# Kernel optimization log

Hardware: AMD Instinct MI355X
Metric: run time of the kernel (lower is better)

## Reference

```python
import jax, jax.numpy as jnp
import numpy as np

MASK_VALUE = -1000000000.0
N = 100000        # num nodes
E = 1600000       # num edges
IN_DIM = 128
HID = 128
MAXN = 100000     # max_num_nodes
TAU = 0.5


def setup_inputs() -> dict:
    key = jax.random.key(0)
    ks = jax.random.split(key, 24)
    s_in = 1.0 / np.sqrt(IN_DIM)
    s_h = 1.0 / np.sqrt(HID)
    s_2h = 1.0 / np.sqrt(2 * HID)
    return {
        "x": jax.random.normal(ks[0], (N, IN_DIM), jnp.float32),
        "edge_index": jax.random.randint(ks[1], (2, E), 0, N, jnp.int32),
        # GCN layer params (PyG GCNConv: lin weight + bias)
        "W1": jax.random.normal(ks[2], (IN_DIM, HID), jnp.float32) * s_in,
        "b1": jnp.zeros((HID,), jnp.float32),
        "W2": jax.random.normal(ks[3], (HID, HID), jnp.float32) * s_h,
        "b2": jnp.zeros((HID,), jnp.float32),
        "W3": jax.random.normal(ks[4], (HID, HID), jnp.float32) * s_h,
        "b3": jnp.zeros((HID,), jnp.float32),
        # heads
        "n1W": jax.random.normal(ks[5], (2 * HID, MAXN), jnp.float32) * s_2h,
        "n1b": jnp.zeros((MAXN,), jnp.float32),
        "n2W": jax.random.normal(ks[6], (2 * HID, MAXN), jnp.float32) * s_2h,
        "n2b": jnp.zeros((MAXN,), jnp.float32),
        "eW": jax.random.normal(ks[7], (2 * HID, 3), jnp.float32) * s_2h,
        "eb": jnp.zeros((3,), jnp.float32),
        "sW": jax.random.normal(ks[8], (2 * HID, 1), jnp.float32) * s_2h,
        "sb": jnp.zeros((1,), jnp.float32),
        # gumbel noise for the 4 gumbel_softmax calls (deterministic reference)
        "g1": jax.random.gumbel(ks[9], (1, MAXN), jnp.float32),
        "g2": jax.random.gumbel(ks[10], (1, MAXN), jnp.float32),
        "ge": jax.random.gumbel(ks[11], (1, 3), jnp.float32),
        "gs": jax.random.gumbel(ks[12], (1, 1), jnp.float32),
    }


def _gcn_layer(x, W, b, src, dst, n):
    # PyG GCNConv: self-loops + symmetric norm D^-1/2 (A+I) D^-1/2 (XW) + b
    h = x @ W                                            # [n, H]
    deg = jnp.zeros((n,), h.dtype).at[dst].add(1.0) + 1.0  # +1 self-loop
    dinv = jax.lax.rsqrt(deg)
    msg = h[src] * (dinv[src] * dinv[dst])[:, None]      # [E, H] gather
    out = jax.ops.segment_sum(msg, dst, num_segments=n)  # scatter-add at targets
    out = out + h * (dinv * dinv)[:, None]               # self-loop contribution
    return out + b


def _gumbel_softmax(logits, g):
    return jax.nn.softmax((logits + g) / TAU, axis=-1)


def _mask_logits(logits, n, prev_idx, src, dst):
    # logits: [1, MAXN]
    idx = jnp.arange(logits.shape[-1])
    logits = jnp.where(idx[None, :] >= n, MASK_VALUE, logits)
    if prev_idx is not None:
        m = (src == prev_idx) | (dst == prev_idx)
        conn = jnp.zeros((logits.shape[-1],), bool)
        # scatter True at connected nodes; unmatched edges map onto prev_idx
        conn = conn.at[jnp.where(m, src, prev_idx)].set(True)
        conn = conn.at[jnp.where(m, dst, prev_idx)].set(True)
        conn = conn.at[prev_idx].set(True)
        logits = jnp.where(conn[None, :], MASK_VALUE, logits)
    return logits


def reference(x, edge_index, W1, b1, W2, b2, W3, b3, n1W, n1b, n2W, n2b, eW, eb, sW, sb, g1, g2, ge, gs):
    src, dst = edge_index[0], edge_index[1]
    n = x.shape[0]
    h = jax.nn.relu(_gcn_layer(x, W1, b1, src, dst, n))
    h = jax.nn.relu(_gcn_layer(h, W2, b2, src, dst, n))
    gcn = jax.nn.relu(_gcn_layer(h, W3, b3, src, dst, n))   # [n, H]

    pool = jnp.concatenate([gcn.mean(0, keepdims=True), gcn.max(0, keepdims=True)], axis=1)  # [1, 2H]

    l1 = _mask_logits(pool @ n1W + n1b, n, None, src, dst)
    n1_soft = _gumbel_softmax(l1, g1)                      # [1, MAXN]
    i1 = jnp.argmax(n1_soft, axis=-1)[0]

    l2 = _mask_logits(pool @ n2W + n2b, n, i1, src, dst)
    n2_soft = _gumbel_softmax(l2, g2)
    i2 = jnp.argmax(n2_soft, axis=-1)[0]

    node_emb = jnp.concatenate([gcn[i1][None, :], gcn[i2][None, :]], axis=1)  # [1, 2H]
    e_soft = _gumbel_softmax(node_emb @ eW + eb, ge)       # [1, 3]
    s_soft = _gumbel_softmax(pool @ sW + sb, gs)           # [1, 1]
    return (n1_soft, n2_soft, e_soft, s_soft)
```

## Files before the change

kernel.cpp:

```cpp
#include <hip/hip_runtime.h>

#define HID 128
#define MASKV -1000000000.0f
#define INV_TAU 2.0f
#define NB_SHIFT 9
#define NBMAX 256
#define ECHUNK 4096
#define FP8_SCALE 16.0f
#define FP8_INV_SCALE 0.0625f

using short8 = __attribute__((ext_vector_type(8))) short;
using f32x4  = __attribute__((ext_vector_type(4))) float;
using f32x2  = __attribute__((ext_vector_type(2))) float;

__device__ inline ushort f2bf(float f) {
  unsigned u = __float_as_uint(f);
  return (ushort)((u + 0x7FFFu + ((u >> 16) & 1u)) >> 16);
}
__device__ inline float bflo(unsigned u) { return __uint_as_float(u << 16); }
__device__ inline float bfhi(unsigned u) { return __uint_as_float(u & 0xFFFF0000u); }

__device__ inline unsigned char f2fp8(float v) {
  int p = __builtin_amdgcn_cvt_pk_fp8_f32(v, v, 0, false);
  return (unsigned char)(p & 0xFF);
}
__device__ inline void acc_fp8x4(unsigned w, float& a0, float& a1, float& a2, float& a3) {
  f32x2 lo = __builtin_amdgcn_cvt_pk_f32_fp8((int)w, false);
  f32x2 hi = __builtin_amdgcn_cvt_pk_f32_fp8((int)w, true);
  a0 += lo[0]; a1 += lo[1]; a2 += hi[0]; a3 += hi[1];
}

__device__ inline unsigned ordered_bits(float f) {
  unsigned u = __float_as_uint(f);
  return (u & 0x80000000u) ? ~u : (u | 0x80000000u);
}
__device__ inline int key_idx(unsigned long long k) {
  return (int)(0xFFFFFFFFu - (unsigned)(k & 0xFFFFFFFFull));
}

__global__ __launch_bounds__(256) void zerok(uint4* __restrict__ p, int n16) {
  int i = blockIdx.x * 256 + threadIdx.x;
  if (i < n16) p[i] = make_uint4(0u, 0u, 0u, 0u);
}

__global__ __launch_bounds__(256) void cvt_w(const float* __restrict__ W1, const float* __restrict__ W2,
                                             const float* __restrict__ W3, ushort* __restrict__ Wt) {
  const float* W = (blockIdx.y == 0) ? W1 : (blockIdx.y == 1) ? W2 : W3;
  ushort* o = Wt + (size_t)blockIdx.y * 128 * 128;
  int idx = blockIdx.x * 256 + threadIdx.x;
  int c = idx >> 7, k = idx & 127;
  o[idx] = f2bf(W[k * 128 + c]);
}

__global__ __launch_bounds__(256) void bucket_count(const int* __restrict__ dst, int E, int* __restrict__ bcnt) {
  __shared__ int h[NBMAX];
  int t = threadIdx.x;
  h[t] = 0;
  __syncthreads();
  for (long long i = (long long)blockIdx.x * 256 + t; i < E; i += (long long)gridDim.x * 256) {
    atomicAdd(&h[dst[i] >> NB_SHIFT], 1);
  }
  __syncthreads();
  if (h[t]) atomicAdd(&bcnt[t], h[t]);
}

__global__ __launch_bounds__(256) void bucket_scan(const int* __restrict__ bcnt, int* __restrict__ bbase,
                                                   int* __restrict__ bcur, int nb, int E) {
  __shared__ int sh[256];
  int t = threadIdx.x;
  int v = (t < nb) ? bcnt[t] : 0;
  sh[t] = v;
  __syncthreads();
  for (int d = 1; d < 256; d <<= 1) {
    int x = (t >= d) ? sh[t - d] : 0;
    __syncthreads();
    sh[t] += x;
    __syncthreads();
  }
  int excl = sh[t] - v;
  if (t < nb) { bbase[t] = excl; bcur[t] = excl; }
  if (t == 0) bbase[nb] = E;
}

__global__ __launch_bounds__(256) void edge_bucket(const int* __restrict__ ei, int E, int nb,
                                                   int* __restrict__ bcur, int2* __restrict__ staged) {
  __shared__ int ssrc[ECHUNK];
  __shared__ int sdst[ECHUNK];
  __shared__ int hist[NBMAX];
  __shared__ int cur[NBMAX];
  int t = threadIdx.x;
  int e0 = blockIdx.x * ECHUNK;
  int cnt = min(ECHUNK, E - e0);
  if (t < nb) hist[t] = 0;
  __syncthreads();
  for (int i = t; i < cnt; i += 256) {
    ssrc[i] = ei[e0 + i];
    int d = ei[E + e0 + i];
    sdst[i] = d;
    atomicAdd(&hist[d >> NB_SHIFT], 1);
  }
  __syncthreads();
  if (t < nb) cur[t] = atomicAdd(&bcur[t], hist[t]);
  __syncthreads();
  for (int i = t; i < cnt; i += 256) {
    int d = sdst[i];
    int pos = atomicAdd(&cur[d >> NB_SHIFT], 1);
    staged[pos] = make_int2(ssrc[i], d);
  }
}

__global__ __launch_bounds__(512) void bucket_csr2(const int2* __restrict__ staged, const int* __restrict__ bbase,
                                                   int* __restrict__ rows, int* __restrict__ cnt,
                                                   float* __restrict__ dinv, int* __restrict__ col, int n) {
  __shared__ int lcnt[512];
  __shared__ int lgs[512];
  __shared__ int lcur[512];
  __shared__ int lsc[512];
  int b = blockIdx.x;
  int t = threadIdx.x;
  int base = b << NB_SHIFT;
  lcnt[t] = 0;
  lcur[t] = 0;
  __syncthreads();
  int start = bbase[b];
  int end = bbase[b + 1];
  for (int i = start + t; i < end; i += 512) {
    atomicAdd(&lcnt[staged[i].y - base], 1);
  }
  __syncthreads();
  int v = lcnt[t];
  lsc[t] = v;
  __syncthreads();
  for (int d = 1; d < 512; d <<= 1) {
    int x = (t >= d) ? lsc[t - d] : 0;
    __syncthreads();
    lsc[t] += x;
    __syncthreads();
  }
  int gstart = start + lsc[t] - v;
  lgs[t] = gstart;
  int node = base + t;
  if (node < n) {
    rows[node] = gstart;
    cnt[node] = v;
    dinv[node] = rsqrtf((float)v + 1.0f);
  }
  __syncthreads();
  for (int i = start + t; i < end; i += 512) {
    int2 p = staged[i];
    int dl = p.y - base;
    int pos = atomicAdd(&lcur[dl], 1);
    col[lgs[dl] + pos] = p.x;
  }
}

template <int F32IN>
__global__ __launch_bounds__(256) void mfma_gemm(const void* __restrict__ Ain, const ushort* __restrict__ Wt,
                                                 const float* __restrict__ dinv, unsigned char* __restrict__ hW8, int n) {
  int w = threadIdx.x >> 6;
  int l = threadIdx.x & 63;
  int lr = l & 15;
  int lg = l >> 4;
  int r0 = blockIdx.x * 64 + w * 16;
  if (r0 >= n) return;
  int arow = r0 + lr;
  if (arow >= n) arow = n - 1;

  f32x4 acc[8];
#pragma unroll
  for (int ct = 0; ct < 8; ++ct) acc[ct] = (f32x4){0.f, 0.f, 0.f, 0.f};

#pragma unroll
  for (int kk = 0; kk < 4; ++kk) {
    short8 a;
    if (F32IN) {
      const float* Af = (const float*)Ain + (size_t)arow * 128 + kk * 32 + lg * 8;
      float4 f0 = ((const float4*)Af)[0];
      float4 f1 = ((const float4*)Af)[1];
      a[0] = (short)f2bf(f0.x); a[1] = (short)f2bf(f0.y);
      a[2] = (short)f2bf(f0.z); a[3] = (short)f2bf(f0.w);
      a[4] = (short)f2bf(f1.x); a[5] = (short)f2bf(f1.y);
      a[6] = (short)f2bf(f1.z); a[7] = (short)f2bf(f1.w);
    } else {
      a = ((const short8*)((const ushort*)Ain + (size_t)arow * 128))[kk * 4 + lg];
    }
#pragma unroll
    for (int ct = 0; ct < 8; ++ct) {
      short8 bfrag = ((const short8*)(Wt + (size_t)(ct * 16 + lr) * 128))[kk * 4 + lg];
      acc[ct] = __builtin_amdgcn_mfma_f32_16x16x32_bf16(a, bfrag, acc[ct], 0, 0, 0);
    }
  }

#pragma unroll
  for (int r = 0; r < 4; ++r) {
    int row = r0 + lg * 4 + r;
    if (row < n) {
      float dv = dinv[row] * FP8_SCALE;
#pragma unroll
      for (int ct = 0; ct < 8; ++ct) {
        hW8[(size_t)row * 128 + ct * 16 + lr] = f2fp8(acc[ct][r] * dv);
      }
    }
  }
}

__global__ __launch_bounds__(256) void gather_k(const int* __restrict__ row_start, const int* __restrict__ cnt,
                                                const int* __restrict__ col, const unsigned char* __restrict__ hW8,
                                                const float* __restrict__ dinv, const float* __restrict__ bias,
                                                ushort* __restrict__ outp, int n) {
  int g = (blockIdx.x * 256 + threadIdx.x) >> 5;
  if (g >= n) return;
  int lane = threadIdx.x & 31;
  const unsigned* h32 = (const unsigned*)hW8;
  float a0 = 0.f, a1 = 0.f, a2 = 0.f, a3 = 0.f;
  acc_fp8x4(h32[(size_t)g * 32 + lane], a0, a1, a2, a3);
  int jb = row_start[g];
  int je = jb + cnt[g];
  int j = jb;
  for (; j + 4 <= je; j += 4) {
    int s0 = __builtin_nontemporal_load(col + j);
    int s1 = __builtin_nontemporal_load(col + j + 1);
    int s2 = __builtin_nontemporal_load(col + j + 2);
    int s3 = __builtin_nontemporal_load(col + j + 3);
    unsigned w0 = h32[(size_t)s0 * 32 + lane];
    unsigned w1 = h32[(size_t)s1 * 32 + lane];
    unsigned w2 = h32[(size_t)s2 * 32 + lane];
    unsigned w3 = h32[(size_t)s3 * 32 + lane];
    acc_fp8x4(w0, a0, a1, a2, a3);
    acc_fp8x4(w1, a0, a1, a2, a3);
    acc_fp8x4(w2, a0, a1, a2, a3);
    acc_fp8x4(w3, a0, a1, a2, a3);
  }
  for (; j < je; ++j) {
    int s0 = __builtin_nontemporal_load(col + j);
    unsigned w0 = h32[(size_t)s0 * 32 + lane];
    acc_fp8x4(w0, a0, a1, a2, a3);
  }
  float din = dinv[g] * FP8_INV_SCALE;
  float4 bb = ((const float4*)bias)[lane];
  a0 = fmaxf(fmaf(a0, din, bb.x), 0.f);
  a1 = fmaxf(fmaf(a1, din, bb.y), 0.f);
  a2 = fmaxf(fmaf(a2, din, bb.z), 0.f);
  a3 = fmaxf(fmaf(a3, din, bb.w), 0.f);
  ushort4 o = {f2bf(a0), f2bf(a1), f2bf(a2), f2bf(a3)};
  *(ushort4*)(outp + (size_t)g * 128 + lane * 4) = o;
}

#define POOL_GRID 512
__global__ __launch_bounds__(256) void pool_kernel(const ushort* __restrict__ gcn, float* __restrict__ psum,
                                                   float* __restrict__ pmax, int nrows) {
  __shared__ float ls[16 * 128];
  __shared__ float lm[16 * 128];
  int t = threadIdx.x;
  int g = t >> 4;
  int c = t & 15;
  float s0 = 0.f, s1 = 0.f, s2 = 0.f, s3 = 0.f, s4 = 0.f, s5 = 0.f, s6 = 0.f, s7 = 0.f;
  float m0 = 0.f, m1 = 0.f, m2 = 0.f, m3 = 0.f, m4 = 0.f, m5 = 0.f, m6 = 0.f, m7 = 0.f;
  for (int r = blockIdx.x * 16 + g; r < nrows; r += POOL_GRID * 16) {
    uint4 w = *(const uint4*)(gcn + (size_t)r * 128 + c * 8);
    float v0 = bflo(w.x), v1 = bfhi(w.x), v2 = bflo(w.y), v3 = bfhi(w.y);
    float v4 = bflo(w.z), v5 = bfhi(w.z), v6 = bflo(w.w), v7 = bfhi(w.w);
    s0 += v0; s1 += v1; s2 += v2; s3 += v3; s4 += v4; s5 += v5; s6 += v6; s7 += v7;
    m0 = fmaxf(m0, v0); m1 = fmaxf(m1, v1); m2 = fmaxf(m2, v2); m3 = fmaxf(m3, v3);
    m4 = fmaxf(m4, v4); m5 = fmaxf(m5, v5); m6 = fmaxf(m6, v6); m7 = fmaxf(m7, v7);
  }
  int cb = c * 8;
  ls[g * 128 + cb + 0] = s0; ls[g * 128 + cb + 1] = s1; ls[g * 128 + cb + 2] = s2; ls[g * 128 + cb + 3] = s3;
  ls[g * 128 + cb + 4] = s4; ls[g * 128 + cb + 5] = s5; ls[g * 128 + cb + 6] = s6; ls[g * 128 + cb + 7] = s7;
  lm[g * 128 + cb + 0] = m0; lm[g * 128 + cb + 1] = m1; lm[g * 128 + cb + 2] = m2; lm[g * 128 + cb + 3] = m3;
  lm[g * 128 + cb + 4] = m4; lm[g * 128 + cb + 5] = m5; lm[g * 128 + cb + 6] = m6; lm[g * 128 + cb + 7] = m7;
  __syncthreads();
  if (t < 128) {
    float s = 0.f, m = 0.f;
#pragma unroll
    for (int gg = 0; gg < 16; ++gg) {
      s += ls[gg * 128 + t];
      m = fmaxf(m, lm[gg * 128 + t]);
    }
    atomicAdd(&psum[t], s);
    atomicMax((unsigned*)&pmax[t], __float_as_uint(m));
  }
}

__global__ __launch_bounds__(256) void head_fused(const float* __restrict__ W, const float* __restrict__ bias,
                                                  const float* __restrict__ g, const float* __restrict__ psum,
                                                  const float* __restrict__ pmax, float invn,
                                                  const int* __restrict__ conn, int use_conn,
                                                  float* __restrict__ ebuf, unsigned long long* __restrict__ cell,
                                                  float* __restrict__ sum, int maxn, int n) {
  __shared__ float p[256];
  __shared__ unsigned long long kred[256];
  __shared__ float sred[256];
  int t = threadIdx.x;
  p[t] = (t < 128) ? psum[t] * invn : pmax[t - 128];
  __syncthreads();
  int j = blockIdx.x * 256 + t;
  unsigned long long key = 0ull;
  float ev = 0.f;
  if (j < maxn) {
    float acc = 0.f;
#pragma unroll 8
    for (int k = 0; k < 256; ++k) acc = fmaf(p[k], W[(size_t)k * maxn + j], acc);
    float logit = acc + bias[j];
    if (j >= n) logit = MASKV;
    if (use_conn && conn[j]) logit = MASKV;
    float zv = (logit + g[j]) * INV_TAU;
    ev = expf(zv);
    ebuf[j] = ev;
    key = ((unsigned long long)ordered_bits(zv) << 32) | (unsigned long long)(0xFFFFFFFFu - (unsigned)j);
  }
  kred[t] = key;
  sred[t] = ev;
  __syncthreads();
  for (int s = 128; s > 0; s >>= 1) {
    if (t < s) {
      kred[t] = kred[t] > kred[t + s] ? kred[t] : kred[t + s];
      sred[t] += sred[t + s];
    }
    __syncthreads();
  }
  if (t == 0) {
    atomicMax(cell, kred[0]);
    atomicAdd(sum, sred[0]);
  }
}

__global__ __launch_bounds__(256) void norm2(const float* __restrict__ e1, const float* __restrict__ s1,
                                             const float* __restrict__ e2, const float* __restrict__ s2,
                                             float* __restrict__ out, int maxn) {
  int j = blockIdx.x * 256 + threadIdx.x;
  if (j < maxn) {
    out[j] = e1[j] / (*s1);
    out[maxn + j] = e2[j] / (*s2);
  }
}

__global__ __launch_bounds__(256) void conn_kernel(const int* __restrict__ ei, int E,
                                                   const unsigned long long* __restrict__ cell1,
                                                   int* __restrict__ conn) {
  int e = blockIdx.x * 256 + threadIdx.x;
  int i1 = key_idx(*cell1);
  if (e == 0) conn[i1] = 1;
  if (e < E) {
    int s = ei[e], d = ei[E + e];
    if (s == i1 || d == i1) {
      conn[s] = 1;
      conn[d] = 1;
    }
  }
}

__global__ __launch_bounds__(128) void edge_head(const ushort* __restrict__ gcn, const float* __restrict__ eW,
                                                 const float* __restrict__ ebias, const float* __restrict__ ge,
                                                 const unsigned long long* __restrict__ c1,
                                                 const unsigned long long* __restrict__ c2,
                                                 float* __restrict__ out_base) {
  __shared__ float red[3 * 128];
  int t = threadIdx.x;
  int i1 = key_idx(*c1);
  int i2 = key_idx(*c2);
  float ea  = __uint_as_float((unsigned)gcn[(size_t)i1 * HID + t] << 16);
  float eb2 = __uint_as_float((unsigned)gcn[(size_t)i2 * HID + t] << 16);
  float p0 = ea * eW[t * 3 + 0] + eb2 * eW[(128 + t) * 3 + 0];
  float p1 = ea * eW[t * 3 + 1] + eb2 * eW[(128 + t) * 3 + 1];
  float p2 = ea * eW[t * 3 + 2] + eb2 * eW[(128 + t) * 3 + 2];
  red[t] = p0; red[128 + t] = p1; red[256 + t] = p2;
  __syncthreads();
  for (int s = 64; s > 0; s >>= 1) {
    if (t < s) {
      red[t] += red[t + s];
      red[128 + t] += red[128 + t + s];
      red[256 + t] += red[256 + t + s];
    }
    __syncthreads();
  }
  if (t == 0) {
    float z0 = (red[0]   + ebias[0] + ge[0]) * INV_TAU;
    float z1 = (red[128] + ebias[1] + ge[1]) * INV_TAU;
    float z2 = (red[256] + ebias[2] + ge[2]) * INV_TAU;
    float m = fmaxf(z0, fmaxf(z1, z2));
    float e0 = expf(z0 - m), e1 = expf(z1 - m), e2 = expf(z2 - m);
    float inv = 1.f / (e0 + e1 + e2);
    out_base[0] = e0 * inv;
    out_base[1] = e1 * inv;
    out_base[2] = e2 * inv;
    out_base[3] = 1.0f;
  }
}

extern "C" void kernel_launch(void* const* d_in, const int* in_sizes, int n_in,
                              void* d_out, int out_size, void* d_ws, size_t ws_size,
                              hipStream_t stream) {
  const float* x  = (const float*)d_in[0];
  const int* ei   = (const int*)d_in[1];
  const float* W1 = (const float*)d_in[2];
  const float* b1 = (const float*)d_in[3];
  const float* W2 = (const float*)d_in[4];
  const float* b2 = (const float*)d_in[5];
  const float* W3 = (const float*)d_in[6];
  const float* b3 = (const float*)d_in[7];
  const float* n1W = (const float*)d_in[8];
  const float* n1b = (const float*)d_in[9];
  const float* n2W = (const float*)d_in[10];
  const float* n2b = (const float*)d_in[11];
  const float* eW  = (const float*)d_in[12];
  const float* eb  = (const float*)d_in[13];
  const float* g1  = (const float*)d_in[16];
  const float* g2  = (const float*)d_in[17];
  const float* ge  = (const float*)d_in[18];

  int n    = in_sizes[0] / HID;
  int E    = in_sizes[1] / 2;
  int maxn = in_sizes[9];
  int nb   = (n + (1 << NB_SHIFT) - 1) >> NB_SHIFT;
  float* out = (float*)d_out;

  char* ws = (char*)d_ws;
  size_t o = 0;
  ushort* H1B = (ushort*)(ws + o); o += (size_t)n * HID * 2;
  ushort* H2B = (ushort*)(ws + o); o += (size_t)n * HID * 2;
  unsigned char* HW8 = (unsigned char*)(ws + o); o += (size_t)n * HID;
  ushort* GCN = (ushort*)(ws + o); o += (size_t)n * HID * 2;
  ushort* WT  = (ushort*)(ws + o); o += (size_t)3 * 128 * 128 * 2;
  float* EB1  = (float*)(ws + o);  o += (size_t)maxn * 4;
  float* EB2  = (float*)(ws + o);  o += (size_t)maxn * 4;
  int* ROWS   = (int*)(ws + o);    o += (size_t)n * 4;
  int* CNT    = (int*)(ws + o);    o += (size_t)n * 4;
  int* COL    = (int*)(ws + o);    o += (size_t)E * 4;
  int2* STAGED = (int2*)(ws + o);  o += (size_t)E * 8;
  float* DINV = (float*)(ws + o);  o += (size_t)n * 4;
  int* BBASE  = (int*)(ws + o);    o += 1040;
  int* BCUR   = (int*)(ws + o);    o += 1024;
  char* zero_start = ws + o;
  int* BCNT   = (int*)(ws + o);    o += 1024;
  int* CONN   = (int*)(ws + o);    o += (size_t)maxn * 4;
  float* PS   = (float*)(ws + o);  o += 128 * 4;
  float* PM   = (float*)(ws + o);  o += 128 * 4;
  unsigned long long* CELLS = (unsigned long long*)(ws + o);
  float* SUM1 = (float*)(ws + o + 16);
  float* SUM2 = (float*)(ws + o + 20);
  o += 64;
  size_t zero_bytes = (size_t)((ws + o) - zero_start);
  int zero16 = (int)(zero_bytes / 16);

  dim3 blk(256);
  int gE = (E + 255) / 256;
  int gHead = (maxn + 255) / 256;
  int gGemm = (n + 63) / 64;
  int gGather = (int)(((size_t)n * 32 + 255) / 256);
  int gEB = (E + ECHUNK - 1) / ECHUNK;
  float invn = 1.0f / (float)n;

  zerok<<<(zero16 + 255) / 256, blk, 0, stream>>>((uint4*)zero_start, zero16);

  cvt_w<<<dim3(64, 3), blk, 0, stream>>>(W1, W2, W3, WT);

  bucket_count<<<1024, blk, 0, stream>>>(ei + E, E, BCNT);
  bucket_scan<<<1, blk, 0, stream>>>(BCNT, BBASE, BCUR, nb, E);

  edge_bucket<<<gEB, blk, 0, stream>>>(ei, E, nb, BCUR, STAGED);
  bucket_csr2<<<nb, dim3(512), 0, stream>>>(STAGED, BBASE, ROWS, CNT, DINV, COL, n);

  mfma_gemm<1><<<gGemm, blk, 0, stream>>>(x, WT, DINV, HW8, n);
  gather_k<<<gGather, blk, 0, stream>>>(ROWS, CNT, COL, HW8, DINV, b1, H1B, n);
  mfma_gemm<0><<<gGemm, blk, 0, stream>>>(H1B, WT + 128 * 128, DINV, HW8, n);
  gather_k<<<gGather, blk, 0, stream>>>(ROWS, CNT, COL, HW8, DINV, b2, H2B, n);
  mfma_gemm<0><<<gGemm, blk, 0, stream>>>(H2B, WT + 2 * 128 * 128, DINV, HW8, n);
  gather_k<<<gGather, blk, 0, stream>>>(ROWS, CNT, COL, HW8, DINV, b3, GCN, n);

  pool_kernel<<<POOL_GRID, blk, 0, stream>>>(GCN, PS, PM, n);

  head_fused<<<gHead, blk, 0, stream>>>(n1W, n1b, g1, PS, PM, invn, nullptr, 0, EB1, &CELLS[0], SUM1, maxn, n);

  conn_kernel<<<gE, blk, 0, stream>>>(ei, E, &CELLS[0], CONN);

  head_fused<<<gHead, blk, 0, stream>>>(n2W, n2b, g2, PS, PM, invn, CONN, 1, EB2, &CELLS[1], SUM2, maxn, n);

  norm2<<<gHead, blk, 0, stream>>>(EB1, SUM1, EB2, SUM2, out, maxn);

  edge_head<<<1, dim3(128), 0, stream>>>(GCN, eW, eb, ge, &CELLS[0], &CELLS[1], out + 2 * (size_t)maxn);
}
```

Before: 456.3 us.

## Merge prep kernels, use fixed-capacity buckets, and widen the head kernel

Folds zeroing, weight conversion and bucket-cursor init into one prep kernel. Bucket counting and scanning are dropped by giving each bucket a fixed BCAP-slot region. norm2 and edge_head are merged into one finish kernel. head_fused now computes two columns per thread with nontemporal weight loads. Fewer launches and no counting pass over edges, but a bucket with more than BCAP edges would overflow.

```diff
diff --git a/kernel.cpp b/kernel.cpp
--- a/kernel.cpp
+++ b/kernel.cpp
@@ -6,6 +6,7 @@
 #define NB_SHIFT 9
 #define NBMAX 256
 #define ECHUNK 4096
+#define BCAP 10240
 #define FP8_SCALE 16.0f
 #define FP8_INV_SCALE 0.0625f
 
@@ -38,48 +39,22 @@
   return (int)(0xFFFFFFFFu - (unsigned)(k & 0xFFFFFFFFull));
 }
 
-__global__ __launch_bounds__(256) void zerok(uint4* __restrict__ p, int n16) {
-  int i = blockIdx.x * 256 + threadIdx.x;
-  if (i < n16) p[i] = make_uint4(0u, 0u, 0u, 0u);
-}
-
-__global__ __launch_bounds__(256) void cvt_w(const float* __restrict__ W1, const float* __restrict__ W2,
-                                             const float* __restrict__ W3, ushort* __restrict__ Wt) {
-  const float* W = (blockIdx.y == 0) ? W1 : (blockIdx.y == 1) ? W2 : W3;
-  ushort* o = Wt + (size_t)blockIdx.y * 128 * 128;
-  int idx = blockIdx.x * 256 + threadIdx.x;
+__global__ __launch_bounds__(256) void prep(uint4* __restrict__ zp, int n16, int* __restrict__ bcur, int zb,
+                                            const float* __restrict__ W1, const float* __restrict__ W2,
+                                            const float* __restrict__ W3, ushort* __restrict__ Wt) {
+  int b = blockIdx.x, t = threadIdx.x;
+  if (b == 0) { bcur[t] = t * BCAP; return; }
+  if (b <= zb) {
+    int i = (b - 1) * 256 + t;
+    if (i < n16) zp[i] = make_uint4(0u, 0u, 0u, 0u);
+    return;
+  }
+  int cb = b - zb - 1;
+  const float* W = (cb < 64) ? W1 : (cb < 128) ? W2 : W3;
+  ushort* o = Wt + (size_t)(cb >> 6) * 128 * 128;
+  int idx = (cb & 63) * 256 + t;
   int c = idx >> 7, k = idx & 127;
   o[idx] = f2bf(W[k * 128 + c]);
-}
-
-__global__ __launch_bounds__(256) void bucket_count(const int* __restrict__ dst, int E, int* __restrict__ bcnt) {
-  __shared__ int h[NBMAX];
-  int t = threadIdx.x;
-  h[t] = 0;
-  __syncthreads();
-  for (long long i = (long long)blockIdx.x * 256 + t; i < E; i += (long long)gridDim.x * 256) {
-    atomicAdd(&h[dst[i] >> NB_SHIFT], 1);
-  }
-  __syncthreads();
-  if (h[t]) atomicAdd(&bcnt[t], h[t]);
-}
-
-__global__ __launch_bounds__(256) void bucket_scan(const int* __restrict__ bcnt, int* __restrict__ bbase,
-                                                   int* __restrict__ bcur, int nb, int E) {
-  __shared__ int sh[256];
-  int t = threadIdx.x;
-  int v = (t < nb) ? bcnt[t] : 0;
-  sh[t] = v;
-  __syncthreads();
-  for (int d = 1; d < 256; d <<= 1) {
-    int x = (t >= d) ? sh[t - d] : 0;
-    __syncthreads();
-    sh[t] += x;
-    __syncthreads();
-  }
-  int excl = sh[t] - v;
-  if (t < nb) { bbase[t] = excl; bcur[t] = excl; }
-  if (t == 0) bbase[nb] = E;
 }
 
 __global__ __launch_bounds__(256) void edge_bucket(const int* __restrict__ ei, int E, int nb,
@@ -109,7 +84,7 @@
   }
 }
 
-__global__ __launch_bounds__(512) void bucket_csr2(const int2* __restrict__ staged, const int* __restrict__ bbase,
+__global__ __launch_bounds__(512) void bucket_csr2(const int2* __restrict__ staged, const int* __restrict__ bcur,
                                                    int* __restrict__ rows, int* __restrict__ cnt,
                                                    float* __restrict__ dinv, int* __restrict__ col, int n) {
   __shared__ int lcnt[512];
@@ -122,8 +97,8 @@
   lcnt[t] = 0;
   lcur[t] = 0;
   __syncthreads();
-  int start = bbase[b];
-  int end = bbase[b + 1];
+  int start = b * BCAP;
+  int end = bcur[b];
   for (int i = start + t; i < end; i += 512) {
     atomicAdd(&lcnt[staged[i].y - base], 1);
   }
@@ -294,23 +269,44 @@
   int t = threadIdx.x;
   p[t] = (t < 128) ? psum[t] * invn : pmax[t - 128];
   __syncthreads();
-  int j = blockIdx.x * 256 + t;
+  int j0 = blockIdx.x * 512 + t;
+  int j1 = j0 + 256;
+  bool v0 = j0 < maxn, v1 = j1 < maxn;
+  float acc0 = 0.f, acc1 = 0.f;
+#pragma unroll 8
+  for (int k = 0; k < 256; ++k) {
+    const float* row = W + (size_t)k * maxn;
+    float w0 = v0 ? __builtin_nontemporal_load(row + j0) : 0.f;
+    float w1 = v1 ? __builtin_nontemporal_load(row + j1) : 0.f;
+    acc0 = fmaf(p[k], w0, acc0);
+    acc1 = fmaf(p[k], w1, acc1);
+  }
   unsigned long long key = 0ull;
-  float ev = 0.f;
-  if (j < maxn) {
-    float acc = 0.f;
-#pragma unroll 8
-    for (int k = 0; k < 256; ++k) acc = fmaf(p[k], W[(size_t)k * maxn + j], acc);
-    float logit = acc + bias[j];
-    if (j >= n) logit = MASKV;
-    if (use_conn && conn[j]) logit = MASKV;
-    float zv = (logit + g[j]) * INV_TAU;
-    ev = expf(zv);
-    ebuf[j] = ev;
-    key = ((unsigned long long)ordered_bits(zv) << 32) | (unsigned long long)(0xFFFFFFFFu - (unsigned)j);
+  float evs = 0.f;
+  if (v0) {
+    float logit = acc0 + bias[j0];
+    if (j0 >= n) logit = MASKV;
+    if (use_conn && conn[j0]) logit = MASKV;
+    float zv = (logit + g[j0]) * INV_TAU;
+    float ev = expf(zv);
+    ebuf[j0] = ev;
+    evs += ev;
+    unsigned long long k0 = ((unsigned long long)ordered_bits(zv) << 32) | (unsigned long long)(0xFFFFFFFFu - (unsigned)j0);
+    key = k0;
+  }
+  if (v1) {
+    float logit = acc1 + bias[j1];
+    if (j1 >= n) logit = MASKV;
+    if (use_conn && conn[j1]) logit = MASKV;
+    float zv = (logit + g[j1]) * INV_TAU;
+    float ev = expf(zv);
+    ebuf[j1] = ev;
+    evs += ev;
+    unsigned long long k1 = ((unsigned long long)ordered_bits(zv) << 32) | (unsigned long long)(0xFFFFFFFFu - (unsigned)j1);
+    key = key > k1 ? key : k1;
   }
   kred[t] = key;
-  sred[t] = ev;
+  sred[t] = evs;
   __syncthreads();
   for (int s = 128; s > 0; s >>= 1) {
     if (t < s) {
@@ -322,16 +318,6 @@
   if (t == 0) {
     atomicMax(cell, kred[0]);
     atomicAdd(sum, sred[0]);
-  }
-}
-
-__global__ __launch_bounds__(256) void norm2(const float* __restrict__ e1, const float* __restrict__ s1,
-                                             const float* __restrict__ e2, const float* __restrict__ s2,
-                                             float* __restrict__ out, int maxn) {
-  int j = blockIdx.x * 256 + threadIdx.x;
-  if (j < maxn) {
-    out[j] = e1[j] / (*s1);
-    out[maxn + j] = e2[j] / (*s2);
   }
 }
 
@@ -350,21 +336,21 @@
   }
 }
 
-__global__ __launch_bounds__(128) void edge_head(const ushort* __restrict__ gcn, const float* __restrict__ eW,
-                                                 const float* __restrict__ ebias, const float* __restrict__ ge,
-                                                 const unsigned long long* __restrict__ c1,
-                                                 const unsigned long long* __restrict__ c2,
-                                                 float* __restrict__ out_base) {
+__device__ void edge_stop(const ushort* __restrict__ gcn, const float* __restrict__ eW,
+                          const float* __restrict__ ebias, const float* __restrict__ ge,
+                          const unsigned long long* __restrict__ c1, const unsigned long long* __restrict__ c2,
+                          float* __restrict__ ob) {
   __shared__ float red[3 * 128];
   int t = threadIdx.x;
-  int i1 = key_idx(*c1);
-  int i2 = key_idx(*c2);
-  float ea  = __uint_as_float((unsigned)gcn[(size_t)i1 * HID + t] << 16);
-  float eb2 = __uint_as_float((unsigned)gcn[(size_t)i2 * HID + t] << 16);
-  float p0 = ea * eW[t * 3 + 0] + eb2 * eW[(128 + t) * 3 + 0];
-  float p1 = ea * eW[t * 3 + 1] + eb2 * eW[(128 + t) * 3 + 1];
-  float p2 = ea * eW[t * 3 + 2] + eb2 * eW[(128 + t) * 3 + 2];
-  red[t] = p0; red[128 + t] = p1; red[256 + t] = p2;
+  if (t < 128) {
+    int i1 = key_idx(*c1);
+    int i2 = key_idx(*c2);
+    float ea  = __uint_as_float((unsigned)gcn[(size_t)i1 * HID + t] << 16);
+    float eb2 = __uint_as_float((unsigned)gcn[(size_t)i2 * HID + t] << 16);
+    red[t]       = ea * eW[t * 3 + 0] + eb2 * eW[(128 + t) * 3 + 0];
+    red[128 + t] = ea * eW[t * 3 + 1] + eb2 * eW[(128 + t) * 3 + 1];
+    red[256 + t] = ea * eW[t * 3 + 2] + eb2 * eW[(128 + t) * 3 + 2];
+  }
   __syncthreads();
   for (int s = 64; s > 0; s >>= 1) {
     if (t < s) {
@@ -381,10 +367,28 @@
     float m = fmaxf(z0, fmaxf(z1, z2));
     float e0 = expf(z0 - m), e1 = expf(z1 - m), e2 = expf(z2 - m);
     float inv = 1.f / (e0 + e1 + e2);
-    out_base[0] = e0 * inv;
-    out_base[1] = e1 * inv;
-    out_base[2] = e2 * inv;
-    out_base[3] = 1.0f;
+    ob[0] = e0 * inv;
+    ob[1] = e1 * inv;
+    ob[2] = e2 * inv;
+    ob[3] = 1.0f;
+  }
+}
+
+__global__ __launch_bounds__(256) void finish(const float* __restrict__ e1, const float* __restrict__ s1,
+                                              const float* __restrict__ e2, const float* __restrict__ s2,
+                                              float* __restrict__ out, int maxn,
+                                              const ushort* __restrict__ gcn, const float* __restrict__ eW,
+                                              const float* __restrict__ ebias, const float* __restrict__ ge,
+                                              const unsigned long long* __restrict__ c1,
+                                              const unsigned long long* __restrict__ c2) {
+  if (blockIdx.x == gridDim.x - 1) {
+    edge_stop(gcn, eW, ebias, ge, c1, c2, out + 2 * (size_t)maxn);
+    return;
+  }
+  int j = blockIdx.x * 256 + threadIdx.x;
+  if (j < maxn) {
+    out[j] = e1[j] / (*s1);
+    out[maxn + j] = e2[j] / (*s2);
   }
 }
 
@@ -426,13 +430,11 @@
   float* EB2  = (float*)(ws + o);  o += (size_t)maxn * 4;
   int* ROWS   = (int*)(ws + o);    o += (size_t)n * 4;
   int* CNT    = (int*)(ws + o);    o += (size_t)n * 4;
-  int* COL    = (int*)(ws + o);    o += (size_t)E * 4;
-  int2* STAGED = (int2*)(ws + o);  o += (size_t)E * 8;
+  int* COL    = (int*)(ws + o);    o += (size_t)NBMAX * BCAP * 4;
+  int2* STAGED = (int2*)(ws + o);  o += (size_t)NBMAX * BCAP * 8;
   float* DINV = (float*)(ws + o);  o += (size_t)n * 4;
-  int* BBASE  = (int*)(ws + o);    o += 1040;
   int* BCUR   = (int*)(ws + o);    o += 1024;
   char* zero_start = ws + o;
-  int* BCNT   = (int*)(ws + o);    o += 1024;
   int* CONN   = (int*)(ws + o);    o += (size_t)maxn * 4;
   float* PS   = (float*)(ws + o);  o += 128 * 4;
   float* PM   = (float*)(ws + o);  o += 128 * 4;
@@ -442,24 +444,21 @@
   o += 64;
   size_t zero_bytes = (size_t)((ws + o) - zero_start);
   int zero16 = (int)(zero_bytes / 16);
+  int zb = (zero16 + 255) / 256;
 
   dim3 blk(256);
   int gE = (E + 255) / 256;
-  int gHead = (maxn + 255) / 256;
+  int gHeadHalf = (maxn + 511) / 512;
+  int gNorm = (maxn + 255) / 256;
   int gGemm = (n + 63) / 64;
   int gGather = (int)(((size_t)n * 32 + 255) / 256);
   int gEB = (E + ECHUNK - 1) / ECHUNK;
   float invn = 1.0f / (float)n;
 
-  zerok<<<(zero16 + 255) / 256, blk, 0, stream>>>((uint4*)zero_start, zero16);
-
-  cvt_w<<<dim3(64, 3), blk, 0, stream>>>(W1, W2, W3, WT);
-
-  bucket_count<<<1024, blk, 0, stream>>>(ei + E, E, BCNT);
-  bucket_scan<<<1, blk, 0, stream>>>(BCNT, BBASE, BCUR, nb, E);
+  prep<<<1 + zb + 192, blk, 0, stream>>>((uint4*)zero_start, zero16, BCUR, zb, W1, W2, W3, WT);
 
   edge_bucket<<<gEB, blk, 0, stream>>>(ei, E, nb, BCUR, STAGED);
-  bucket_csr2<<<nb, dim3(512), 0, stream>>>(STAGED, BBASE, ROWS, CNT, DINV, COL, n);
+  bucket_csr2<<<nb, dim3(512), 0, stream>>>(STAGED, BCUR, ROWS, CNT, DINV, COL, n);
 
   mfma_gemm<1><<<gGemm, blk, 0, stream>>>(x, WT, DINV, HW8, n);
   gather_k<<<gGather, blk, 0, stream>>>(ROWS, CNT, COL, HW8, DINV, b1, H1B, n);
@@ -470,13 +469,11 @@
 
   pool_kernel<<<POOL_GRID, blk, 0, stream>>>(GCN, PS, PM, n);
 
-  head_fused<<<gHead, blk, 0, stream>>>(n1W, n1b, g1, PS, PM, invn, nullptr, 0, EB1, &CELLS[0], SUM1, maxn, n);
+  head_fused<<<gHeadHalf, blk, 0, stream>>>(n1W, n1b, g1, PS, PM, invn, nullptr, 0, EB1, &CELLS[0], SUM1, maxn, n);
 
   conn_kernel<<<gE, blk, 0, stream>>>(ei, E, &CELLS[0], CONN);
 
-  head_fused<<<gHead, blk, 0, stream>>>(n2W, n2b, g2, PS, PM, invn, CONN, 1, EB2, &CELLS[1], SUM2, maxn, n);
-
-  norm2<<<gHead, blk, 0, stream>>>(EB1, SUM1, EB2, SUM2, out, maxn);
-
-  edge_head<<<1, dim3(128), 0, stream>>>(GCN, eW, eb, ge, &CELLS[0], &CELLS[1], out + 2 * (size_t)maxn);
-}
+  head_fused<<<gHeadHalf, blk, 0, stream>>>(n2W, n2b, g2, PS, PM, invn, CONN, 1, EB2, &CELLS[1], SUM2, maxn, n);
+
+  finish<<<gNorm + 1, blk, 0, stream>>>(EB1, SUM1, EB2, SUM2, out, maxn, GCN, eW, eb, ge, &CELLS[0], &CELLS[1]);
+}
```

Result: faster. 408.1 us (-10.6%).
